# Kernel tuning notes

Measured on AMD Instinct MI355X. Metric: run time of the kernel, lower is better.

The kernel has to match this reference:

```python
import jax, jax.numpy as jnp
import numpy as np

N, E, B = 30000, 60000, 500          # nodes, edges, graphs
NODE_IN, EDGE_IN, H, R = 64, 16, 64, 1024
MP_STEPS, S2S_STEPS = 3, 3           # num_step_message_passing, num_step_set2set
D = 2 * H                            # Set2Set in_channels / LSTM hidden size


def setup_inputs() -> dict:
    key = jax.random.key(0)
    ks = jax.random.split(key, 20)
    g = lambda i, shape, s: jax.random.normal(ks[i], shape, jnp.float32) * s
    return {
        "x": g(0, (N, NODE_IN), 1.0),
        "edge_index": jax.random.randint(ks[1], (2, E), 0, N),
        "edge_attr": g(2, (E, EDGE_IN), 1.0),
        "batch": jnp.sort(jax.random.randint(ks[3], (N,), 0, B)),
        # project_node_feats
        "W_proj": g(4, (NODE_IN, H), 0.1), "b_proj": jnp.zeros((H,), jnp.float32),
        # NNConv edge network + root + bias
        "W_edge": g(5, (EDGE_IN, H * H), 0.05), "b_edge": jnp.zeros((H * H,), jnp.float32),
        "root": g(6, (H, H), 0.1), "conv_bias": jnp.zeros((H,), jnp.float32),
        # GRU (torch gate order r, z, n)
        "gru_W_ih": g(7, (3 * H, H), 0.1), "gru_W_hh": g(8, (3 * H, H), 0.1),
        "gru_b_ih": jnp.zeros((3 * H,), jnp.float32), "gru_b_hh": jnp.zeros((3 * H,), jnp.float32),
        # node classifier head
        "W_cls": g(9, (H, 1), 0.1), "b_cls": jnp.zeros((1,), jnp.float32),
        # Set2Set LSTM: input 2D (=4H), hidden D (=2H), gate order i, f, g, o
        "lstm_W_ih": g(10, (4 * D, 2 * D), 0.1), "lstm_W_hh": g(11, (4 * D, D), 0.1),
        "lstm_b_ih": jnp.zeros((4 * D,), jnp.float32), "lstm_b_hh": jnp.zeros((4 * D,), jnp.float32),
        # sparsify (Linear 4H->R + PReLU)
        "W_sp": g(12, (4 * H, R), 0.05), "b_sp": jnp.zeros((R,), jnp.float32),
        "prelu_a": jnp.float32(0.25),
        "W_y1": g(13, (R, 128), 0.05), "b_y1": jnp.zeros((128,), jnp.float32),
        "W_y2": g(14, (128, 1), 0.1), "b_y2": jnp.zeros((1,), jnp.float32),
    }


def reference(x, edge_index, edge_attr, batch,
              W_proj, b_proj, W_edge, b_edge, root, conv_bias,
              gru_W_ih, gru_W_hh, gru_b_ih, gru_b_hh,
              W_cls, b_cls,
              lstm_W_ih, lstm_W_hh, lstm_b_ih, lstm_b_hh,
              W_sp, b_sp, prelu_a, W_y1, b_y1, W_y2, b_y2):
    src, dst = edge_index[0], edge_index[1]
    h0 = jax.nn.relu(x @ W_proj + b_proj)                  # [N, H]
    # Per-edge HxH weight matrices (loop-invariant; NNConv recomputes same values).
    We = (edge_attr @ W_edge + b_edge).reshape(E, H, H)    # [E, H, H]

    node, hidden = h0, h0
    for _ in range(MP_STEPS):
        msg = jnp.einsum('eh,eho->eo', node[src], We)      # gather + per-edge matvec
        aggr = jax.ops.segment_sum(msg, dst, num_segments=N)
        m = jax.nn.relu(aggr + node @ root + conv_bias)    # NNConv output + activation
        # GRU cell (seq_len=1)
        gi = m @ gru_W_ih.T + gru_b_ih
        gh = hidden @ gru_W_hh.T + gru_b_hh
        r = jax.nn.sigmoid(gi[:, :H] + gh[:, :H])
        z = jax.nn.sigmoid(gi[:, H:2 * H] + gh[:, H:2 * H])
        n = jnp.tanh(gi[:, 2 * H:] + r * gh[:, 2 * H:])
        hidden = (1.0 - z) * n + z * hidden
        node = hidden

    xcat = jnp.concatenate([h0, node], axis=1)             # [N, 2H] = [N, D]
    p_borylation = (node @ W_cls + b_cls)[:, 0]            # [N]

    # Set2Set over xcat
    q_star = jnp.zeros((B, 2 * D), xcat.dtype)
    hs = jnp.zeros((B, D), xcat.dtype)
    cs = jnp.zeros((B, D), xcat.dtype)
    for _ in range(S2S_STEPS):
        gts = q_star @ lstm_W_ih.T + lstm_b_ih + hs @ lstm_W_hh.T + lstm_b_hh
        i_g = jax.nn.sigmoid(gts[:, :D])
        f_g = jax.nn.sigmoid(gts[:, D:2 * D])
        g_g = jnp.tanh(gts[:, 2 * D:3 * D])
        o_g = jax.nn.sigmoid(gts[:, 3 * D:])
        cs = f_g * cs + i_g * g_g
        hs = o_g * jnp.tanh(cs)
        q = hs                                             # [B, D]
        e = jnp.sum(xcat * q[batch], axis=-1)              # [N]
        mseg = jax.ops.segment_max(e, batch, num_segments=B)
        ex = jnp.exp(e - mseg[batch])
        denom = jax.ops.segment_sum(ex, batch, num_segments=B)
        a = ex / denom[batch]                              # segment softmax
        rvec = jax.ops.segment_sum(a[:, None] * xcat, batch, num_segments=B)
        q_star = jnp.concatenate([q, rvec], axis=1)        # [B, 2D] = [B, 4H]

    gf = q_star @ W_sp + b_sp
    gf = jnp.where(gf >= 0, gf, prelu_a * gf)              # PReLU
    predicted_yield = (jax.nn.relu(gf @ W_y1 + b_y1) @ W_y2 + b_y2)[:, 0]
    return p_borylation, predicted_yield
```

## Files before the change

kernel.cpp:

```cpp
#include <hip/hip_runtime.h>
#include <math.h>

#define NN 30000
#define NNP 30080
#define NE 60000
#define NB 500
#define YGH 256
#define KE 1088

typedef __attribute__((ext_vector_type(8))) short bf16x8;
typedef __attribute__((ext_vector_type(4))) float f32x4;

__device__ __forceinline__ float sigmoidf_(float x) { return 1.0f / (1.0f + expf(-x)); }

__device__ __forceinline__ unsigned short bf_hi(float x) {
  unsigned int u = __float_as_uint(x);
  u += 0x7FFF + ((u >> 16) & 1);
  return (unsigned short)(u >> 16);
}
__device__ __forceinline__ float bf_f(unsigned short h) {
  return __uint_as_float(((unsigned int)h) << 16);
}
__device__ __forceinline__ void split_bf(float x, unsigned short& hi, unsigned short& lo) {
  hi = bf_hi(x);
  lo = bf_hi(x - bf_f(hi));
}

__device__ __forceinline__ int lower_bound_i(const int* __restrict__ a, int n, int v) {
  int lo = 0, hi = n;
  while (lo < hi) { int mid = (lo + hi) >> 1; if (a[mid] < v) lo = mid + 1; else hi = mid; }
  return lo;
}

__global__ __launch_bounds__(256) void gemm_mfma_k(
    const unsigned short* __restrict__ Ahi, const unsigned short* __restrict__ Alo,
    const unsigned short* __restrict__ Bhi, const unsigned short* __restrict__ Blo,
    float* __restrict__ C, int ldc,
    float* __restrict__ C2,
    unsigned short* __restrict__ Chi, unsigned short* __restrict__ Clo,
    const float* __restrict__ bias, int M, int flags)
{
  const int tid = threadIdx.x;
  const int wid = tid >> 6, lane = tid & 63;
  const int l15 = lane & 15, l4 = lane >> 4;
  const int r0 = blockIdx.x * 128 + (wid >> 1) * 64;
  const int c0 = blockIdx.y * 64 + (wid & 1) * 32;

  f32x4 acc[4][2];
#pragma unroll
  for (int rt = 0; rt < 4; rt++)
#pragma unroll
    for (int ct = 0; ct < 2; ct++) acc[rt][ct] = (f32x4){0.f, 0.f, 0.f, 0.f};

#pragma unroll
  for (int ks = 0; ks < 2; ks++) {
    const int kb = ks * 32 + l4 * 8;
    bf16x8 a_h[4], a_l[4], b_h[2], b_l[2];
#pragma unroll
    for (int rt = 0; rt < 4; rt++) {
      size_t off = (size_t)(r0 + rt * 16 + l15) * 64 + kb;
      a_h[rt] = *(const bf16x8*)(Ahi + off);
      a_l[rt] = *(const bf16x8*)(Alo + off);
    }
#pragma unroll
    for (int ct = 0; ct < 2; ct++) {
      size_t off = (size_t)(c0 + ct * 16 + l15) * 64 + kb;
      b_h[ct] = *(const bf16x8*)(Bhi + off);
      b_l[ct] = *(const bf16x8*)(Blo + off);
    }
#pragma unroll
    for (int rt = 0; rt < 4; rt++)
#pragma unroll
      for (int ct = 0; ct < 2; ct++) {
        acc[rt][ct] = __builtin_amdgcn_mfma_f32_16x16x32_bf16(a_h[rt], b_h[ct], acc[rt][ct], 0, 0, 0);
        acc[rt][ct] = __builtin_amdgcn_mfma_f32_16x16x32_bf16(a_h[rt], b_l[ct], acc[rt][ct], 0, 0, 0);
        acc[rt][ct] = __builtin_amdgcn_mfma_f32_16x16x32_bf16(a_l[rt], b_h[ct], acc[rt][ct], 0, 0, 0);
      }
  }

#pragma unroll
  for (int rt = 0; rt < 4; rt++) {
    const int rbase = r0 + rt * 16 + l4 * 4;
#pragma unroll
    for (int ct = 0; ct < 2; ct++) {
      const int col = c0 + ct * 16 + l15;
      const float bv = (flags & 1) ? bias[col] : 0.f;
#pragma unroll
      for (int reg = 0; reg < 4; reg++) {
        const int row = rbase + reg;
        if (row < M) {
          float v = acc[rt][ct][reg];
          if (flags & 1) v = fmaxf(v + bv, 0.f);
          C[(size_t)row * ldc + col] = v;
          if (flags & 4) C2[(size_t)row * 64 + col] = v;
          if (flags & 2) {
            unsigned short h, l;
            split_bf(v, h, l);
            Chi[(size_t)row * 64 + col] = h;
            Clo[(size_t)row * 64 + col] = l;
          }
        }
      }
    }
  }
}

__global__ __launch_bounds__(256) void edge_mfma_k(
    const int* __restrict__ ei, const float* __restrict__ ea,
    const float* __restrict__ h,
    const unsigned short* __restrict__ Whi, const unsigned short* __restrict__ Wlo,
    float* __restrict__ Yb)
{
  const int tid = threadIdx.x;
  const int wid = tid >> 6, lane = tid & 63;
  const int l15 = lane & 15, l4 = lane >> 4;
  const int e0 = (blockIdx.x * 4 + wid) * 64;

  int srcA[4];
  const float* eaA[4];
#pragma unroll
  for (int rt = 0; rt < 4; rt++) {
    int e = e0 + rt * 16 + l15;
    int ee = (e < NE) ? e : (NE - 1);
    srcA[rt] = ei[ee];
    eaA[rt] = ea + (size_t)ee * 16;
  }

  f32x4 acc[4][4];
#pragma unroll
  for (int rt = 0; rt < 4; rt++)
#pragma unroll
    for (int ct = 0; ct < 4; ct++) acc[rt][ct] = (f32x4){0.f, 0.f, 0.f, 0.f};

  for (int ks = 0; ks < KE / 32; ks++) {
    const int base = ks * 32 + l4 * 8;
    const int c = base >> 6;
    const int kb = base & 63;
    bf16x8 ah[4], al[4];
#pragma unroll
    for (int rt = 0; rt < 4; rt++) {
      float eac = (c < 16) ? eaA[rt][c] : 1.0f;
      const float* hp = h + (size_t)srcA[rt] * 64 + kb;
      float4 n0 = *(const float4*)hp;
      float4 n1 = *(const float4*)(hp + 4);
      float nv[8] = {n0.x, n0.y, n0.z, n0.w, n1.x, n1.y, n1.z, n1.w};
#pragma unroll
      for (int j = 0; j < 8; j++) {
        unsigned short hb, lb;
        split_bf(eac * nv[j], hb, lb);
        ah[rt][j] = (short)hb;
        al[rt][j] = (short)lb;
      }
    }
#pragma unroll
    for (int ct = 0; ct < 4; ct++) {
      size_t wo = (size_t)(ct * 16 + l15) * KE + base;
      bf16x8 bh = *(const bf16x8*)(Whi + wo);
      bf16x8 bl = *(const bf16x8*)(Wlo + wo);
#pragma unroll
      for (int rt = 0; rt < 4; rt++) {
        acc[rt][ct] = __builtin_amdgcn_mfma_f32_16x16x32_bf16(ah[rt], bh, acc[rt][ct], 0, 0, 0);
        acc[rt][ct] = __builtin_amdgcn_mfma_f32_16x16x32_bf16(ah[rt], bl, acc[rt][ct], 0, 0, 0);
        acc[rt][ct] = __builtin_amdgcn_mfma_f32_16x16x32_bf16(al[rt], bh, acc[rt][ct], 0, 0, 0);
      }
    }
  }

#pragma unroll
  for (int rt = 0; rt < 4; rt++) {
    const int er = e0 + rt * 16 + l4 * 4;
#pragma unroll
    for (int reg = 0; reg < 4; reg++) {
      const int e = er + reg;
      if (e < NE) {
        const int dst = ei[NE + e];
#pragma unroll
        for (int ct = 0; ct < 4; ct++)
          atomicAdd(&Yb[(size_t)dst * YGH + ct * 16 + l15], acc[rt][ct][reg]);
      }
    }
  }
}

__global__ __launch_bounds__(256) void prep_bt_k(
    const float* __restrict__ W_edge, const float* __restrict__ b_edge,
    const float* __restrict__ root, const float* __restrict__ gWhh,
    const float* __restrict__ gWih, const float* __restrict__ W_proj,
    unsigned short* __restrict__ BTbig_hi, unsigned short* __restrict__ BTbig_lo,
    unsigned short* __restrict__ W2_hi, unsigned short* __restrict__ W2_lo,
    unsigned short* __restrict__ BTih_hi, unsigned short* __restrict__ BTih_lo,
    unsigned short* __restrict__ BTp_hi, unsigned short* __restrict__ BTp_lo)
{
  int idx = blockIdx.x * 256 + threadIdx.x;
  const int NBIG = YGH * 64, NW2 = 64 * KE, NIH = 192 * 64, NP = 64 * 64;
  if (idx < NBIG) {
    int col = idx >> 6, k = idx & 63;
    float v = (col < 64) ? root[k * 64 + col] : gWhh[(size_t)(col - 64) * 64 + k];
    unsigned short h, l; split_bf(v, h, l);
    BTbig_hi[idx] = h; BTbig_lo[idx] = l;
  } else if (idx < NBIG + NW2) {
    int i2 = idx - NBIG;
    int o2 = i2 / KE, kq = i2 % KE;
    int c = kq >> 6, kk = kq & 63;
    float v = (c < 16) ? W_edge[(size_t)c * 4096 + kk * 64 + o2] : b_edge[kk * 64 + o2];
    unsigned short h, l; split_bf(v, h, l);
    W2_hi[i2] = h; W2_lo[i2] = l;
  } else if (idx < NBIG + NW2 + NIH) {
    int i2 = idx - NBIG - NW2;
    float v = gWih[i2];
    unsigned short h, l; split_bf(v, h, l);
    BTih_hi[i2] = h; BTih_lo[i2] = l;
  } else if (idx < NBIG + NW2 + NIH + NP) {
    int i2 = idx - NBIG - NW2 - NIH;
    int o2 = i2 >> 6, k = i2 & 63;
    float v = W_proj[k * 64 + o2];
    unsigned short h, l; split_bf(v, h, l);
    BTp_hi[i2] = h; BTp_lo[i2] = l;
  }
}

__global__ __launch_bounds__(256) void prep_lstmT_k(
    const float* __restrict__ Wih, const float* __restrict__ Whh,
    float* __restrict__ Tih, float* __restrict__ Thh)
{
  int idx = blockIdx.x * 256 + threadIdx.x;
  if (idx < 256 * 512) {
    int j = idx / 512, r = idx % 512;
    Tih[idx] = Wih[(size_t)r * 256 + j];
  } else if (idx < 256 * 512 + 128 * 512) {
    int id2 = idx - 256 * 512;
    int j = id2 / 512, r = id2 % 512;
    Thh[id2] = Whh[(size_t)r * 128 + j];
  }
}

__global__ __launch_bounds__(256) void split2_k(
    const float* __restrict__ src, unsigned short* __restrict__ hi,
    unsigned short* __restrict__ lo, int n4)
{
  int i = blockIdx.x * 256 + threadIdx.x;
  if (i >= n4) return;
  float4 v = ((const float4*)src)[i];
  unsigned short h0, l0, h1, l1, h2, l2, h3, l3;
  split_bf(v.x, h0, l0); split_bf(v.y, h1, l1);
  split_bf(v.z, h2, l2); split_bf(v.w, h3, l3);
  ((ushort4*)hi)[i] = make_ushort4(h0, h1, h2, h3);
  ((ushort4*)lo)[i] = make_ushort4(l0, l1, l2, l3);
}

__global__ __launch_bounds__(256) void m_relu_split_k(
    const float* __restrict__ Yb, const float* __restrict__ conv_b,
    unsigned short* __restrict__ mbh, unsigned short* __restrict__ mbl)
{
  int t = blockIdx.x * 256 + threadIdx.x;
  if (t >= NN * 64) return;
  int n = t >> 6, c = t & 63;
  float v = fmaxf(Yb[(size_t)n * YGH + c] + conv_b[c], 0.f);
  unsigned short h, l; split_bf(v, h, l);
  mbh[t] = h; mbl[t] = l;
}

__global__ __launch_bounds__(256) void gru_split_k(
    const float* __restrict__ gi, const float* __restrict__ Yb,
    const float* __restrict__ bih, const float* __restrict__ bhh,
    float* __restrict__ h, unsigned short* __restrict__ hh, unsigned short* __restrict__ hl)
{
  int t = blockIdx.x * 256 + threadIdx.x;
  if (t >= NN * 64) return;
  int n = t >> 6, c = t & 63;
  const float* gin = gi + (size_t)n * 192;
  const float* ghn = Yb + (size_t)n * YGH + 64;
  float r = sigmoidf_(gin[c] + bih[c] + ghn[c] + bhh[c]);
  float z = sigmoidf_(gin[64 + c] + bih[64 + c] + ghn[64 + c] + bhh[64 + c]);
  float ng = tanhf(gin[128 + c] + bih[128 + c] + r * (ghn[128 + c] + bhh[128 + c]));
  float hv = h[t];
  float hn = (1.f - z) * ng + z * hv;
  h[t] = hn;
  unsigned short hb, lb; split_bf(hn, hb, lb);
  hh[t] = hb; hl[t] = lb;
}

__global__ __launch_bounds__(256) void cls_xcat_k(
    const float* __restrict__ h, const float* __restrict__ Wcls,
    const float* __restrict__ bcls, float* __restrict__ xcat, float* __restrict__ out)
{
  int gw = (blockIdx.x * blockDim.x + threadIdx.x) >> 6;
  if (gw >= NN) return;
  int lane = threadIdx.x & 63;
  float hv = h[(size_t)gw * 64 + lane];
  xcat[(size_t)gw * 128 + 64 + lane] = hv;
  float p = hv * Wcls[lane];
#pragma unroll
  for (int off = 32; off > 0; off >>= 1) p += __shfl_xor(p, off);
  if (lane == 0) out[gw] = p + bcls[0];
}

__global__ __launch_bounds__(256) void gemmK_k(
    const float* __restrict__ A, int lda,
    const float* __restrict__ B, int ldb,
    float* __restrict__ C, int ldc,
    const float* __restrict__ Csrc,
    const float* __restrict__ bias, const float* __restrict__ alpha_p,
    int M, int K, int flags)
{
  __shared__ float As[64 * 68];
  __shared__ float Bs[64 * 64];
  const int tid = threadIdx.x;
  const int m0 = blockIdx.x * 64;
  const int n0 = blockIdx.y * 64;
  const int tx = tid & 15, ty = tid >> 4;
  float acc[4][4] = {};

  for (int kc = 0; kc < K; kc += 64) {
#pragma unroll
    for (int i = 0; i < 4; i++) {
      int f4 = tid + i * 256;
      int row = f4 >> 4;
      int kk = (f4 & 15) << 2;
      float4 v = make_float4(0.f, 0.f, 0.f, 0.f);
      if (m0 + row < M) v = *(const float4*)(A + (size_t)(m0 + row) * lda + kc + kk);
      *(float4*)&As[row * 68 + kk] = v;
    }
#pragma unroll
    for (int i = 0; i < 4; i++) {
      int f4 = tid + i * 256;
      int kk = f4 >> 4;
      int nn = (f4 & 15) << 2;
      float4 v = *(const float4*)(B + (size_t)(kc + kk) * ldb + n0 + nn);
      *(float4*)&Bs[kk * 64 + nn] = v;
    }
    __syncthreads();
    const float* As0 = As + (ty * 4 + 0) * 68;
    const float* As1 = As + (ty * 4 + 1) * 68;
    const float* As2 = As + (ty * 4 + 2) * 68;
    const float* As3 = As + (ty * 4 + 3) * 68;
#pragma unroll
    for (int k = 0; k < 64; k++) {
      float4 b = *(const float4*)(Bs + k * 64 + tx * 4);
      float a0 = As0[k], a1 = As1[k], a2 = As2[k], a3 = As3[k];
      acc[0][0] = fmaf(a0, b.x, acc[0][0]); acc[0][1] = fmaf(a0, b.y, acc[0][1]);
      acc[0][2] = fmaf(a0, b.z, acc[0][2]); acc[0][3] = fmaf(a0, b.w, acc[0][3]);
      acc[1][0] = fmaf(a1, b.x, acc[1][0]); acc[1][1] = fmaf(a1, b.y, acc[1][1]);
      acc[1][2] = fmaf(a1, b.z, acc[1][2]); acc[1][3] = fmaf(a1, b.w, acc[1][3]);
      acc[2][0] = fmaf(a2, b.x, acc[2][0]); acc[2][1] = fmaf(a2, b.y, acc[2][1]);
      acc[2][2] = fmaf(a2, b.z, acc[2][2]); acc[2][3] = fmaf(a2, b.w, acc[2][3]);
      acc[3][0] = fmaf(a3, b.x, acc[3][0]); acc[3][1] = fmaf(a3, b.y, acc[3][1]);
      acc[3][2] = fmaf(a3, b.z, acc[3][2]); acc[3][3] = fmaf(a3, b.w, acc[3][3]);
    }
    __syncthreads();
  }

  const int coln = tx * 4;
  const int col = n0 + coln;
  float alpha = (flags & 32) ? alpha_p[0] : 0.f;
#pragma unroll
  for (int i = 0; i < 4; i++) {
    int row = m0 + ty * 4 + i;
    if (row < M) {
      float v0 = acc[i][0], v1 = acc[i][1], v2 = acc[i][2], v3 = acc[i][3];
      size_t off = (size_t)row * ldc + col;
      if (flags & 4) {
        float4 s = *(const float4*)(Csrc + off);
        v0 += s.x; v1 += s.y; v2 += s.z; v3 += s.w;
      }
      if (flags & 1) {
        v0 += bias[col + 0]; v1 += bias[col + 1]; v2 += bias[col + 2]; v3 += bias[col + 3];
      }
      if (flags & 2) {
        v0 = fmaxf(v0, 0.f); v1 = fmaxf(v1, 0.f); v2 = fmaxf(v2, 0.f); v3 = fmaxf(v3, 0.f);
      }
      if (flags & 32) {
        v0 = (v0 >= 0.f) ? v0 : alpha * v0; v1 = (v1 >= 0.f) ? v1 : alpha * v1;
        v2 = (v2 >= 0.f) ? v2 : alpha * v2; v3 = (v3 >= 0.f) ? v3 : alpha * v3;
      }
      *(float4*)&C[off] = make_float4(v0, v1, v2, v3);
    }
  }
}

__global__ __launch_bounds__(256) void lstm_elem_k(
    const float* __restrict__ gts, const float* __restrict__ bih, const float* __restrict__ bhh,
    float* __restrict__ hs, float* __restrict__ cs)
{
  int t = blockIdx.x * 256 + threadIdx.x;
  if (t >= NB * 128) return;
  int b = t >> 7, d = t & 127;
  const float* g = gts + (size_t)b * 512;
  float iv = sigmoidf_(g[d] + bih[d] + bhh[d]);
  float fv = sigmoidf_(g[128 + d] + bih[128 + d] + bhh[128 + d]);
  float gv = tanhf(g[256 + d] + bih[256 + d] + bhh[256 + d]);
  float ov = sigmoidf_(g[384 + d] + bih[384 + d] + bhh[384 + d]);
  float c = fv * cs[t] + iv * gv;
  cs[t] = c;
  hs[t] = ov * tanhf(c);
}

__global__ __launch_bounds__(256) void attn_k(
    const float* __restrict__ xcat, const int* __restrict__ batch,
    const float* __restrict__ hs, float* __restrict__ e_ws, float* __restrict__ q_star)
{
  __shared__ float q[128];
  __shared__ float red[4];
  __shared__ float rvw[4 * 128];
  __shared__ float dw[4];
  __shared__ int se[2];
  int b = blockIdx.x;
  int tid = threadIdx.x;
  if (tid < 128) q[tid] = hs[(size_t)b * 128 + tid];
  if (tid == 254) se[0] = lower_bound_i(batch, NN, b);
  if (tid == 255) se[1] = lower_bound_i(batch, NN, b + 1);
  __syncthreads();
  int start = se[0], end = se[1];
  int lane = tid & 63, w = tid >> 6;
  float wmax = -INFINITY;
  for (int n = start + w; n < end; n += 4) {
    const float* xr = xcat + (size_t)n * 128;
    float p = xr[lane] * q[lane] + xr[64 + lane] * q[64 + lane];
#pragma unroll
    for (int off = 32; off > 0; off >>= 1) p += __shfl_xor(p, off);
    if (lane == 0) e_ws[n] = p;
    wmax = fmaxf(wmax, p);
  }
  if (lane == 0) red[w] = wmax;
  __syncthreads();
  float bmax = fmaxf(fmaxf(red[0], red[1]), fmaxf(red[2], red[3]));
  float a0 = 0.f, a1 = 0.f, ds = 0.f;
  for (int n = start + w; n < end; n += 4) {
    float ex = expf(e_ws[n] - bmax);
    const float* xr = xcat + (size_t)n * 128;
    a0 = fmaf(ex, xr[lane], a0);
    a1 = fmaf(ex, xr[64 + lane], a1);
    ds += ex;
  }
  rvw[w * 128 + lane] = a0;
  rvw[w * 128 + 64 + lane] = a1;
  if (lane == 0) dw[w] = ds;
  __syncthreads();
  if (tid < 128) {
    float r = rvw[tid] + rvw[128 + tid] + rvw[256 + tid] + rvw[384 + tid];
    float dsum = dw[0] + dw[1] + dw[2] + dw[3];
    q_star[(size_t)b * 256 + tid] = q[tid];
    q_star[(size_t)b * 256 + 128 + tid] = (end > start) ? (r / dsum) : 0.f;
  }
}

__global__ __launch_bounds__(256) void yout_k(
    const float* __restrict__ y1, const float* __restrict__ Wy2,
    const float* __restrict__ by2, float* __restrict__ out)
{
  int gw = (blockIdx.x * blockDim.x + threadIdx.x) >> 6;
  if (gw >= NB) return;
  int lane = threadIdx.x & 63;
  const float* yr = y1 + (size_t)gw * 128;
  float p = yr[lane] * Wy2[lane] + yr[64 + lane] * Wy2[64 + lane];
#pragma unroll
  for (int off = 32; off > 0; off >>= 1) p += __shfl_xor(p, off);
  if (lane == 0) out[gw] = p + by2[0];
}

extern "C" void kernel_launch(void* const* d_in, const int* in_sizes, int n_in,
                              void* d_out, int out_size, void* d_ws, size_t ws_size,
                              hipStream_t stream) {
  const float* x      = (const float*)d_in[0];
  const int*   ei     = (const int*)d_in[1];
  const float* ea     = (const float*)d_in[2];
  const int*   batch  = (const int*)d_in[3];
  const float* W_proj = (const float*)d_in[4];
  const float* b_proj = (const float*)d_in[5];
  const float* W_edge = (const float*)d_in[6];
  const float* b_edge = (const float*)d_in[7];
  const float* root   = (const float*)d_in[8];
  const float* conv_b = (const float*)d_in[9];
  const float* gWih   = (const float*)d_in[10];
  const float* gWhh   = (const float*)d_in[11];
  const float* gbih   = (const float*)d_in[12];
  const float* gbhh   = (const float*)d_in[13];
  const float* Wcls   = (const float*)d_in[14];
  const float* bcls   = (const float*)d_in[15];
  const float* lWih   = (const float*)d_in[16];
  const float* lWhh   = (const float*)d_in[17];
  const float* lbih   = (const float*)d_in[18];
  const float* lbhh   = (const float*)d_in[19];
  const float* Wsp    = (const float*)d_in[20];
  const float* bsp    = (const float*)d_in[21];
  const float* pa     = (const float*)d_in[22];
  const float* Wy1    = (const float*)d_in[23];
  const float* by1    = (const float*)d_in[24];
  const float* Wy2    = (const float*)d_in[25];
  const float* by2    = (const float*)d_in[26];
  float* out = (float*)d_out;

  float* ws = (float*)d_ws;
  size_t o = 0;
  float* h      = ws + o; o += (size_t)NN * 64;
  float* Ybig   = ws + o; o += (size_t)NN * YGH;
  float* gi     = ws + o; o += (size_t)NN * 192;
  float* xcat   = ws + o; o += (size_t)NN * 128;
  float* e_ws   = ws + o; o += (size_t)NN;
  float* q_star = ws + o; o += (size_t)NB * 256;
  float* hs     = ws + o; o += (size_t)NB * 128;
  float* cs     = ws + o; o += (size_t)NB * 128;
  float* Tih    = ws + o; o += 256 * 512;
  float* Thh    = ws + o; o += 128 * 512;
  float* gts    = ws + o; o += (size_t)NB * 512;
  float* gf     = ws + o; o += (size_t)NB * 1024;
  float* y1     = ws + o; o += (size_t)NB * 128;

  unsigned short* us = (unsigned short*)(ws + o);
  size_t u = 0;
  unsigned short* hh_b   = us + u; u += (size_t)NNP * 64;
  unsigned short* hl_b   = us + u; u += (size_t)NNP * 64;
  unsigned short* mbh    = us + u; u += (size_t)NNP * 64;
  unsigned short* mbl    = us + u; u += (size_t)NNP * 64;
  unsigned short* BTb_hi = us + u; u += (size_t)YGH * 64;
  unsigned short* BTb_lo = us + u; u += (size_t)YGH * 64;
  unsigned short* W2_hi  = us + u; u += (size_t)64 * KE;
  unsigned short* W2_lo  = us + u; u += (size_t)64 * KE;
  unsigned short* BTi_hi = us + u; u += (size_t)192 * 64;
  unsigned short* BTi_lo = us + u; u += (size_t)192 * 64;
  unsigned short* BTp_hi = us + u; u += (size_t)64 * 64;
  unsigned short* BTp_lo = us + u; u += (size_t)64 * 64;

  const int MT = NNP / 128;
  const int ET = (NE + 255) / 256;
  const int PREP_N = YGH * 64 + 64 * KE + 192 * 64 + 64 * 64;

  prep_bt_k<<<(PREP_N + 255) / 256, 256, 0, stream>>>(
      W_edge, b_edge, root, gWhh, gWih, W_proj,
      BTb_hi, BTb_lo, W2_hi, W2_lo, BTi_hi, BTi_lo, BTp_hi, BTp_lo);
  prep_lstmT_k<<<768, 256, 0, stream>>>(lWih, lWhh, Tih, Thh);
  split2_k<<<(NN * 16 + 255) / 256, 256, 0, stream>>>(x, hh_b, hl_b, NN * 16);

  gemm_mfma_k<<<dim3(MT, 1), 256, 0, stream>>>(hh_b, hl_b, BTp_hi, BTp_lo,
                                               xcat, 128, h, hh_b, hl_b, b_proj, NN, 1 | 2 | 4);
  for (int step = 0; step < 3; step++) {
    gemm_mfma_k<<<dim3(MT, YGH / 64), 256, 0, stream>>>(hh_b, hl_b, BTb_hi, BTb_lo,
                                                        Ybig, YGH, nullptr, nullptr, nullptr,
                                                        nullptr, NN, 0);
    edge_mfma_k<<<ET, 256, 0, stream>>>(ei, ea, h, W2_hi, W2_lo, Ybig);
    m_relu_split_k<<<(NN * 64) / 256, 256, 0, stream>>>(Ybig, conv_b, mbh, mbl);
    gemm_mfma_k<<<dim3(MT, 3), 256, 0, stream>>>(mbh, mbl, BTi_hi, BTi_lo,
                                                 gi, 192, nullptr, nullptr, nullptr,
                                                 nullptr, NN, 0);
    gru_split_k<<<(NN * 64) / 256, 256, 0, stream>>>(gi, Ybig, gbih, gbhh, h, hh_b, hl_b);
  }
  cls_xcat_k<<<(NN * 64) / 256, 256, 0, stream>>>(h, Wcls, bcls, xcat, out);
  hipMemsetAsync(q_star, 0, (size_t)NB * (256 + 128 + 128) * sizeof(float), stream);
  for (int t = 0; t < 3; t++) {
    gemmK_k<<<dim3(8, 8), 256, 0, stream>>>(q_star, 256, Tih, 512, gts, 512,
                                            nullptr, nullptr, nullptr, NB, 256, 0);
    gemmK_k<<<dim3(8, 8), 256, 0, stream>>>(hs, 128, Thh, 512, gts, 512,
                                            gts, nullptr, nullptr, NB, 128, 4);
    lstm_elem_k<<<(NB * 128 + 255) / 256, 256, 0, stream>>>(gts, lbih, lbhh, hs, cs);
    attn_k<<<NB, 256, 0, stream>>>(xcat, batch, hs, e_ws, q_star);
  }
  gemmK_k<<<dim3(8, 16), 256, 0, stream>>>(q_star, 256, Wsp, 1024, gf, 1024,
                                           nullptr, bsp, pa, NB, 256, 1 | 32);
  gemmK_k<<<dim3(8, 2), 256, 0, stream>>>(gf, 1024, Wy1, 128, y1, 128,
                                          nullptr, by1, nullptr, NB, 1024, 1 | 2);
  yout_k<<<(NB * 64 + 255) / 256, 256, 0, stream>>>(y1, Wy2, by2, out + NN);
}
```

Measured before the change: 776.2 us.

## Split edge MFMA K-dimension across 4 grid slices and preload source features

The edge kernel's K loop over 17 chunks of 64 (16 edge-attr channels plus a bias chunk) is split across blockIdx.y into four slices of 5/4/4/4 chunks, giving four times as many blocks. Each slice atomically adds its partial sums into Ybig. Each wave now loads its source-node rows of h once into registers instead of reloading them every K step. The bias chunk reads the precomputed bf16 hi/lo split of h rather than re-splitting it. The trade-off is four times as many atomicAdds to Ybig and redundant gathers of h across the slices.

New measurement: 856.9 us. 1.1x slower.

```diff
diff --git a/kernel.cpp b/kernel.cpp
--- a/kernel.cpp
+++ b/kernel.cpp
@@ -108,6 +108,7 @@
 __global__ __launch_bounds__(256) void edge_mfma_k(
     const int* __restrict__ ei, const float* __restrict__ ea,
     const float* __restrict__ h,
+    const unsigned short* __restrict__ hh, const unsigned short* __restrict__ hl,
     const unsigned short* __restrict__ Whi, const unsigned short* __restrict__ Wlo,
     float* __restrict__ Yb)
 {
@@ -115,15 +116,24 @@
   const int wid = tid >> 6, lane = tid & 63;
   const int l15 = lane & 15, l4 = lane >> 4;
   const int e0 = (blockIdx.x * 4 + wid) * 64;
-
-  int srcA[4];
-  const float* eaA[4];
+  const int kb = l4 * 8;
+  const int cs = (blockIdx.y == 0) ? 0 : 5 + (blockIdx.y - 1) * 4;
+  const int ce = 5 + blockIdx.y * 4;
+
+  int srcA[4], eRow[4];
+  float4 hv[4][4];
 #pragma unroll
   for (int rt = 0; rt < 4; rt++) {
     int e = e0 + rt * 16 + l15;
     int ee = (e < NE) ? e : (NE - 1);
-    srcA[rt] = ei[ee];
-    eaA[rt] = ea + (size_t)ee * 16;
+    eRow[rt] = ee;
+    int s = ei[ee];
+    srcA[rt] = s;
+    const float* hp = h + (size_t)s * 64 + kb;
+    hv[rt][0] = *(const float4*)(hp);
+    hv[rt][1] = *(const float4*)(hp + 4);
+    hv[rt][2] = *(const float4*)(hp + 32);
+    hv[rt][3] = *(const float4*)(hp + 36);
   }
 
   f32x4 acc[4][4];
@@ -132,36 +142,44 @@
 #pragma unroll
     for (int ct = 0; ct < 4; ct++) acc[rt][ct] = (f32x4){0.f, 0.f, 0.f, 0.f};
 
-  for (int ks = 0; ks < KE / 32; ks++) {
-    const int base = ks * 32 + l4 * 8;
-    const int c = base >> 6;
-    const int kb = base & 63;
-    bf16x8 ah[4], al[4];
-#pragma unroll
-    for (int rt = 0; rt < 4; rt++) {
-      float eac = (c < 16) ? eaA[rt][c] : 1.0f;
-      const float* hp = h + (size_t)srcA[rt] * 64 + kb;
-      float4 n0 = *(const float4*)hp;
-      float4 n1 = *(const float4*)(hp + 4);
-      float nv[8] = {n0.x, n0.y, n0.z, n0.w, n1.x, n1.y, n1.z, n1.w};
-#pragma unroll
-      for (int j = 0; j < 8; j++) {
-        unsigned short hb, lb;
-        split_bf(eac * nv[j], hb, lb);
-        ah[rt][j] = (short)hb;
-        al[rt][j] = (short)lb;
-      }
-    }
-#pragma unroll
-    for (int ct = 0; ct < 4; ct++) {
-      size_t wo = (size_t)(ct * 16 + l15) * KE + base;
-      bf16x8 bh = *(const bf16x8*)(Whi + wo);
-      bf16x8 bl = *(const bf16x8*)(Wlo + wo);
-#pragma unroll
-      for (int rt = 0; rt < 4; rt++) {
-        acc[rt][ct] = __builtin_amdgcn_mfma_f32_16x16x32_bf16(ah[rt], bh, acc[rt][ct], 0, 0, 0);
-        acc[rt][ct] = __builtin_amdgcn_mfma_f32_16x16x32_bf16(ah[rt], bl, acc[rt][ct], 0, 0, 0);
-        acc[rt][ct] = __builtin_amdgcn_mfma_f32_16x16x32_bf16(al[rt], bh, acc[rt][ct], 0, 0, 0);
+  for (int c = cs; c < ce; c++) {
+#pragma unroll
+    for (int ks = 0; ks < 2; ks++) {
+      bf16x8 ah[4], al[4];
+      if (c < 16) {
+#pragma unroll
+        for (int rt = 0; rt < 4; rt++) {
+          const float eac = ea[(size_t)eRow[rt] * 16 + c];
+          const float4 va = hv[rt][ks * 2], vb = hv[rt][ks * 2 + 1];
+          const float nv[8] = {va.x, va.y, va.z, va.w, vb.x, vb.y, vb.z, vb.w};
+#pragma unroll
+          for (int j = 0; j < 8; j++) {
+            unsigned short hb, lb;
+            split_bf(eac * nv[j], hb, lb);
+            ah[rt][j] = (short)hb;
+            al[rt][j] = (short)lb;
+          }
+        }
+      } else {
+#pragma unroll
+        for (int rt = 0; rt < 4; rt++) {
+          size_t off = (size_t)srcA[rt] * 64 + ks * 32 + kb;
+          ah[rt] = *(const bf16x8*)(hh + off);
+          al[rt] = *(const bf16x8*)(hl + off);
+        }
+      }
+      const int base = c * 64 + ks * 32 + kb;
+#pragma unroll
+      for (int ct = 0; ct < 4; ct++) {
+        size_t wo = (size_t)(ct * 16 + l15) * KE + base;
+        bf16x8 bh = *(const bf16x8*)(Whi + wo);
+        bf16x8 bl = *(const bf16x8*)(Wlo + wo);
+#pragma unroll
+        for (int rt = 0; rt < 4; rt++) {
+          acc[rt][ct] = __builtin_amdgcn_mfma_f32_16x16x32_bf16(ah[rt], bh, acc[rt][ct], 0, 0, 0);
+          acc[rt][ct] = __builtin_amdgcn_mfma_f32_16x16x32_bf16(ah[rt], bl, acc[rt][ct], 0, 0, 0);
+          acc[rt][ct] = __builtin_amdgcn_mfma_f32_16x16x32_bf16(al[rt], bh, acc[rt][ct], 0, 0, 0);
+        }
       }
     }
   }
@@ -537,7 +555,7 @@
     gemm_mfma_k<<<dim3(MT, YGH / 64), 256, 0, stream>>>(hh_b, hl_b, BTb_hi, BTb_lo,
                                                         Ybig, YGH, nullptr, nullptr, nullptr,
                                                         nullptr, NN, 0);
-    edge_mfma_k<<<ET, 256, 0, stream>>>(ei, ea, h, W2_hi, W2_lo, Ybig);
+    edge_mfma_k<<<dim3(ET, 4), 256, 0, stream>>>(ei, ea, h, hh_b, hl_b, W2_hi, W2_lo, Ybig);
     m_relu_split_k<<<(NN * 64) / 256, 256, 0, stream>>>(Ybig, conv_b, mbh, mbl);
     gemm_mfma_k<<<dim3(MT, 3), 256, 0, stream>>>(mbh, mbl, BTi_hi, BTi_lo,
                                                  gi, 192, nullptr, nullptr, nullptr,
```

## Fuse relu-split into GRU input GEMM and merge LSTM weight matrices

Applied to the files above, without the earlier changes.

Removes the separate relu+bf16-split kernel by doing bias, ReLU and hi/lo splitting on the fly inside a dedicated GRU input-gate GEMM that reads Ybig directly. In Set2Set, q equals hs, so W_ih[:, :128] and W_hh are pre-summed into one combined matrix, which drops the second small GEMM per step. The LSTM elementwise update is folded into the attention kernel. Together these cut launches and intermediate traffic. In exchange, the A operand is recomputed per column block (3x), and rounding changes slightly because the two weight matrices are summed before the product.

Result: faster. 717.6 us (-7.5%).

```diff
diff --git a/kernel.cpp b/kernel.cpp
--- a/kernel.cpp
+++ b/kernel.cpp
@@ -100,6 +100,80 @@
             Clo[(size_t)row * 64 + col] = l;
           }
         }
+      }
+    }
+  }
+}
+
+__global__ __launch_bounds__(256) void gi_gemm_k(
+    const float* __restrict__ Yb, const float* __restrict__ conv_b,
+    const unsigned short* __restrict__ Bhi, const unsigned short* __restrict__ Blo,
+    float* __restrict__ gi)
+{
+  const int tid = threadIdx.x;
+  const int wid = tid >> 6, lane = tid & 63;
+  const int l15 = lane & 15, l4 = lane >> 4;
+  const int r0 = blockIdx.x * 128 + (wid >> 1) * 64;
+  const int c0 = blockIdx.y * 64 + (wid & 1) * 32;
+
+  f32x4 acc[4][2];
+#pragma unroll
+  for (int rt = 0; rt < 4; rt++)
+#pragma unroll
+    for (int ct = 0; ct < 2; ct++) acc[rt][ct] = (f32x4){0.f, 0.f, 0.f, 0.f};
+
+#pragma unroll
+  for (int ks = 0; ks < 2; ks++) {
+    const int kb = ks * 32 + l4 * 8;
+    bf16x8 a_h[4], a_l[4], b_h[2], b_l[2];
+    float4 cb0 = *(const float4*)(conv_b + kb);
+    float4 cb1 = *(const float4*)(conv_b + kb + 4);
+    const float cbv[8] = {cb0.x, cb0.y, cb0.z, cb0.w, cb1.x, cb1.y, cb1.z, cb1.w};
+#pragma unroll
+    for (int rt = 0; rt < 4; rt++) {
+      const int row = r0 + rt * 16 + l15;
+      float4 y0 = make_float4(0.f, 0.f, 0.f, 0.f), y1 = y0;
+      if (row < NN) {
+        const float* yp = Yb + (size_t)row * YGH + kb;
+        y0 = *(const float4*)(yp);
+        y1 = *(const float4*)(yp + 4);
+      }
+      const float yv[8] = {y0.x, y0.y, y0.z, y0.w, y1.x, y1.y, y1.z, y1.w};
+#pragma unroll
+      for (int j = 0; j < 8; j++) {
+        float v = fmaxf(yv[j] + cbv[j], 0.f);
+        unsigned short hb_, lb_;
+        split_bf(v, hb_, lb_);
+        a_h[rt][j] = (short)hb_;
+        a_l[rt][j] = (short)lb_;
+      }
+    }
+#pragma unroll
+    for (int ct = 0; ct < 2; ct++) {
+      size_t off = (size_t)(c0 + ct * 16 + l15) * 64 + kb;
+      b_h[ct] = *(const bf16x8*)(Bhi + off);
+      b_l[ct] = *(const bf16x8*)(Blo + off);
+    }
+#pragma unroll
+    for (int rt = 0; rt < 4; rt++)
+#pragma unroll
+      for (int ct = 0; ct < 2; ct++) {
+        acc[rt][ct] = __builtin_amdgcn_mfma_f32_16x16x32_bf16(a_h[rt], b_h[ct], acc[rt][ct], 0, 0, 0);
+        acc[rt][ct] = __builtin_amdgcn_mfma_f32_16x16x32_bf16(a_h[rt], b_l[ct], acc[rt][ct], 0, 0, 0);
+        acc[rt][ct] = __builtin_amdgcn_mfma_f32_16x16x32_bf16(a_l[rt], b_h[ct], acc[rt][ct], 0, 0, 0);
+      }
+  }
+
+#pragma unroll
+  for (int rt = 0; rt < 4; rt++) {
+    const int rbase = r0 + rt * 16 + l4 * 4;
+#pragma unroll
+    for (int ct = 0; ct < 2; ct++) {
+      const int col = c0 + ct * 16 + l15;
+#pragma unroll
+      for (int reg = 0; reg < 4; reg++) {
+        const int row = rbase + reg;
+        if (row < NN) gi[(size_t)row * 192 + col] = acc[rt][ct][reg];
       }
     }
   }
@@ -219,19 +293,15 @@
   }
 }
 
-__global__ __launch_bounds__(256) void prep_lstmT_k(
-    const float* __restrict__ Wih, const float* __restrict__ Whh,
-    float* __restrict__ Tih, float* __restrict__ Thh)
+__global__ __launch_bounds__(256) void prep_tcomb_k(
+    const float* __restrict__ Wih, const float* __restrict__ Whh, float* __restrict__ T)
 {
   int idx = blockIdx.x * 256 + threadIdx.x;
-  if (idx < 256 * 512) {
-    int j = idx / 512, r = idx % 512;
-    Tih[idx] = Wih[(size_t)r * 256 + j];
-  } else if (idx < 256 * 512 + 128 * 512) {
-    int id2 = idx - 256 * 512;
-    int j = id2 / 512, r = id2 % 512;
-    Thh[id2] = Whh[(size_t)r * 128 + j];
-  }
+  if (idx >= 256 * 512) return;
+  int j = idx / 512, r = idx % 512;
+  float v = Wih[(size_t)r * 256 + j];
+  if (j < 128) v += Whh[(size_t)r * 128 + j];
+  T[idx] = v;
 }
 
 __global__ __launch_bounds__(256) void split2_k(
@@ -246,18 +316,6 @@
   split_bf(v.z, h2, l2); split_bf(v.w, h3, l3);
   ((ushort4*)hi)[i] = make_ushort4(h0, h1, h2, h3);
   ((ushort4*)lo)[i] = make_ushort4(l0, l1, l2, l3);
-}
-
-__global__ __launch_bounds__(256) void m_relu_split_k(
-    const float* __restrict__ Yb, const float* __restrict__ conv_b,
-    unsigned short* __restrict__ mbh, unsigned short* __restrict__ mbl)
-{
-  int t = blockIdx.x * 256 + threadIdx.x;
-  if (t >= NN * 64) return;
-  int n = t >> 6, c = t & 63;
-  float v = fmaxf(Yb[(size_t)n * YGH + c] + conv_b[c], 0.f);
-  unsigned short h, l; split_bf(v, h, l);
-  mbh[t] = h; mbl[t] = l;
 }
 
 __global__ __launch_bounds__(256) void gru_split_k(
@@ -378,26 +436,11 @@
   }
 }
 
-__global__ __launch_bounds__(256) void lstm_elem_k(
+__global__ __launch_bounds__(256) void lstm_attn_k(
     const float* __restrict__ gts, const float* __restrict__ bih, const float* __restrict__ bhh,
-    float* __restrict__ hs, float* __restrict__ cs)
-{
-  int t = blockIdx.x * 256 + threadIdx.x;
-  if (t >= NB * 128) return;
-  int b = t >> 7, d = t & 127;
-  const float* g = gts + (size_t)b * 512;
-  float iv = sigmoidf_(g[d] + bih[d] + bhh[d]);
-  float fv = sigmoidf_(g[128 + d] + bih[128 + d] + bhh[128 + d]);
-  float gv = tanhf(g[256 + d] + bih[256 + d] + bhh[256 + d]);
-  float ov = sigmoidf_(g[384 + d] + bih[384 + d] + bhh[384 + d]);
-  float c = fv * cs[t] + iv * gv;
-  cs[t] = c;
-  hs[t] = ov * tanhf(c);
-}
-
-__global__ __launch_bounds__(256) void attn_k(
+    float* __restrict__ cs,
     const float* __restrict__ xcat, const int* __restrict__ batch,
-    const float* __restrict__ hs, float* __restrict__ e_ws, float* __restrict__ q_star)
+    float* __restrict__ e_ws, float* __restrict__ q_star)
 {
   __shared__ float q[128];
   __shared__ float red[4];
@@ -406,7 +449,17 @@
   __shared__ int se[2];
   int b = blockIdx.x;
   int tid = threadIdx.x;
-  if (tid < 128) q[tid] = hs[(size_t)b * 128 + tid];
+  if (tid < 128) {
+    int d = tid;
+    const float* g = gts + (size_t)b * 512;
+    float iv = sigmoidf_(g[d] + bih[d] + bhh[d]);
+    float fv = sigmoidf_(g[128 + d] + bih[128 + d] + bhh[128 + d]);
+    float gv = tanhf(g[256 + d] + bih[256 + d] + bhh[256 + d]);
+    float ov = sigmoidf_(g[384 + d] + bih[384 + d] + bhh[384 + d]);
+    float c = fv * cs[(size_t)b * 128 + d] + iv * gv;
+    cs[(size_t)b * 128 + d] = c;
+    q[d] = ov * tanhf(c);
+  }
   if (tid == 254) se[0] = lower_bound_i(batch, NN, b);
   if (tid == 255) se[1] = lower_bound_i(batch, NN, b + 1);
   __syncthreads();
@@ -498,10 +551,8 @@
   float* xcat   = ws + o; o += (size_t)NN * 128;
   float* e_ws   = ws + o; o += (size_t)NN;
   float* q_star = ws + o; o += (size_t)NB * 256;
-  float* hs     = ws + o; o += (size_t)NB * 128;
   float* cs     = ws + o; o += (size_t)NB * 128;
-  float* Tih    = ws + o; o += 256 * 512;
-  float* Thh    = ws + o; o += 128 * 512;
+  float* Tcomb  = ws + o; o += 256 * 512;
   float* gts    = ws + o; o += (size_t)NB * 512;
   float* gf     = ws + o; o += (size_t)NB * 1024;
   float* y1     = ws + o; o += (size_t)NB * 128;
@@ -510,8 +561,6 @@
   size_t u = 0;
   unsigned short* hh_b   = us + u; u += (size_t)NNP * 64;
   unsigned short* hl_b   = us + u; u += (size_t)NNP * 64;
-  unsigned short* mbh    = us + u; u += (size_t)NNP * 64;
-  unsigned short* mbl    = us + u; u += (size_t)NNP * 64;
   unsigned short* BTb_hi = us + u; u += (size_t)YGH * 64;
   unsigned short* BTb_lo = us + u; u += (size_t)YGH * 64;
   unsigned short* W2_hi  = us + u; u += (size_t)64 * KE;
@@ -528,7 +577,7 @@
   prep_bt_k<<<(PREP_N + 255) / 256, 256, 0, stream>>>(
       W_edge, b_edge, root, gWhh, gWih, W_proj,
       BTb_hi, BTb_lo, W2_hi, W2_lo, BTi_hi, BTi_lo, BTp_hi, BTp_lo);
-  prep_lstmT_k<<<768, 256, 0, stream>>>(lWih, lWhh, Tih, Thh);
+  prep_tcomb_k<<<512, 256, 0, stream>>>(lWih, lWhh, Tcomb);
   split2_k<<<(NN * 16 + 255) / 256, 256, 0, stream>>>(x, hh_b, hl_b, NN * 16);
 
   gemm_mfma_k<<<dim3(MT, 1), 256, 0, stream>>>(hh_b, hl_b, BTp_hi, BTp_lo,
@@ -538,21 +587,15 @@
                                                         Ybig, YGH, nullptr, nullptr, nullptr,
                                                         nullptr, NN, 0);
     edge_mfma_k<<<ET, 256, 0, stream>>>(ei, ea, h, W2_hi, W2_lo, Ybig);
-    m_relu_split_k<<<(NN * 64) / 256, 256, 0, stream>>>(Ybig, conv_b, mbh, mbl);
-    gemm_mfma_k<<<dim3(MT, 3), 256, 0, stream>>>(mbh, mbl, BTi_hi, BTi_lo,
-                                                 gi, 192, nullptr, nullptr, nullptr,
-                                                 nullptr, NN, 0);
+    gi_gemm_k<<<dim3(MT, 3), 256, 0, stream>>>(Ybig, conv_b, BTi_hi, BTi_lo, gi);
     gru_split_k<<<(NN * 64) / 256, 256, 0, stream>>>(gi, Ybig, gbih, gbhh, h, hh_b, hl_b);
   }
   cls_xcat_k<<<(NN * 64) / 256, 256, 0, stream>>>(h, Wcls, bcls, xcat, out);
-  hipMemsetAsync(q_star, 0, (size_t)NB * (256 + 128 + 128) * sizeof(float), stream);
+  hipMemsetAsync(q_star, 0, (size_t)NB * (256 + 128) * sizeof(float), stream);
   for (int t = 0; t < 3; t++) {
-    gemmK_k<<<dim3(8, 8), 256, 0, stream>>>(q_star, 256, Tih, 512, gts, 512,
+    gemmK_k<<<dim3(8, 8), 256, 0, stream>>>(q_star, 256, Tcomb, 512, gts, 512,
                                             nullptr, nullptr, nullptr, NB, 256, 0);
-    gemmK_k<<<dim3(8, 8), 256, 0, stream>>>(hs, 128, Thh, 512, gts, 512,
-                                            gts, nullptr, nullptr, NB, 128, 4);
-    lstm_elem_k<<<(NB * 128 + 255) / 256, 256, 0, stream>>>(gts, lbih, lbhh, hs, cs);
-    attn_k<<<NB, 256, 0, stream>>>(xcat, batch, hs, e_ws, q_star);
+    lstm_attn_k<<<NB, 256, 0, stream>>>(gts, lbih, lbhh, cs, xcat, batch, e_ws, q_star);
   }
   gemmK_k<<<dim3(8, 16), 256, 0, stream>>>(q_star, 256, Wsp, 1024, gf, 1024,
                                            nullptr, bsp, pa, NB, 256, 1 | 32);
```
